# Kernel optimization log

Measured on AMD Instinct MI355X. Metric: run time of the kernel, lower is better.

## Reference

```python
import jax, jax.numpy as jnp
from jax import lax
import numpy as np

N, K, F, H, NG, T = 32768, 16, 64, 128, 1024, 2


def setup_inputs() -> dict:
    key = jax.random.key(0)
    ks = jax.random.split(key, 24)
    def rn(k, shape, s=0.05):
        return jax.random.normal(k, shape, jnp.float32) * s
    inp = {
        'n': jax.random.normal(ks[0], (N, F), jnp.float32),
        'nbr': jax.random.randint(ks[1], (N, K), 0, N),
        # deterministic sorted graph ids -> every graph non-empty (safe segment_max)
        'gid': (jnp.arange(N) * NG) // N,
        'G': NG,
        # SAGEConv layer 1: LSTM(F,F), fc_self/fc_neigh F->H
        'lstm1_Wih': rn(ks[2], (F, 4 * F)), 'lstm1_Whh': rn(ks[3], (F, 4 * F)), 'lstm1_b': jnp.zeros((4 * F,), jnp.float32),
        'fcs1_W': rn(ks[4], (F, H)), 'fcs1_b': jnp.zeros((H,), jnp.float32),
        'fcn1_W': rn(ks[5], (F, H)), 'fcn1_b': jnp.zeros((H,), jnp.float32),
        # SAGEConv layer 2: LSTM(H,H), fc_self/fc_neigh H->H
        'lstm2_Wih': rn(ks[6], (H, 4 * H)), 'lstm2_Whh': rn(ks[7], (H, 4 * H)), 'lstm2_b': jnp.zeros((4 * H,), jnp.float32),
        'fcs2_W': rn(ks[8], (H, H)), 'fcs2_b': jnp.zeros((H,), jnp.float32),
        'fcn2_W': rn(ks[9], (H, H)), 'fcn2_b': jnp.zeros((H,), jnp.float32),
        # WeightedSumAndMax atom weighting: H->1
        'rw_W': rn(ks[10], (H, 1)), 'rw_b': jnp.zeros((1,), jnp.float32),
        # task head: 2H->H, H->T
        'h1_W': rn(ks[11], (2 * H, H)), 'h1_b': jnp.zeros((H,), jnp.float32),
        'h2_W': rn(ks[12], (H, T)), 'h2_b': jnp.zeros((T,), jnp.float32),
    }
    return inp


def _lstm_last(xseq, Wih, Whh, b):
    # xseq: [N, K, Fin]; returns last hidden state [N, Hh]
    Hh = Whh.shape[0]
    h0 = jnp.zeros((xseq.shape[0], Hh), xseq.dtype)
    def step(carry, xt):
        h, c = carry
        g = xt @ Wih + h @ Whh + b  # [N, 4H], torch gate order i,f,g,o
        i, f, gg, o = jnp.split(g, 4, axis=-1)
        c = jax.nn.sigmoid(f) * c + jax.nn.sigmoid(i) * jnp.tanh(gg)
        h = jax.nn.sigmoid(o) * jnp.tanh(c)
        return (h, c), None
    (h, _), _ = lax.scan(step, (h0, h0), jnp.swapaxes(xseq, 0, 1))
    return h


def _sage_layer(x, nbr, Wih, Whh, b, Ws, bs, Wn, bn):
    hn = _lstm_last(x[nbr], Wih, Whh, b)          # LSTM aggregate of neighbors
    return jax.nn.sigmoid(x @ Ws + bs + hn @ Wn + bn)


def reference(n, nbr, gid, G,
              lstm1_Wih, lstm1_Whh, lstm1_b, fcs1_W, fcs1_b, fcn1_W, fcn1_b,
              lstm2_Wih, lstm2_Whh, lstm2_b, fcs2_W, fcs2_b, fcn2_W, fcn2_b,
              rw_W, rw_b, h1_W, h1_b, h2_W, h2_b):
    G = int(G)
    h1 = _sage_layer(n, nbr, lstm1_Wih, lstm1_Whh, lstm1_b, fcs1_W, fcs1_b, fcn1_W, fcn1_b)
    h2 = _sage_layer(h1, nbr, lstm2_Wih, lstm2_Whh, lstm2_b, fcs2_W, fcs2_b, fcn2_W, fcn2_b)
    # WeightedSumAndMax readout
    w = jax.nn.sigmoid(h2 @ rw_W + rw_b)                       # [N,1]
    wsum = jax.ops.segment_sum(w * h2, gid, num_segments=G)    # [G,H]
    mx = jax.ops.segment_max(h2, gid, num_segments=G)          # [G,H]
    gemb = jnp.concatenate([wsum, mx], axis=-1)                # [G,2H]
    y = jax.nn.sigmoid(gemb @ h1_W + h1_b)
    y = jax.nn.sigmoid(y @ h2_W + h2_b)                        # classification
    return y
```

## Files before the change

kernel.cpp:

```cpp
#include <hip/hip_runtime.h>

typedef unsigned short u16;
typedef __attribute__((ext_vector_type(8))) short bf16x8;
typedef __attribute__((ext_vector_type(4))) float f32x4;
typedef __attribute__((ext_vector_type(2))) float f32x2;

constexpr int N_ = 32768;
constexpr int H_ = 128;
constexpr int G_ = 1024;
constexpr int T_ = 2;

__device__ __forceinline__ float sigf(float x){
  float e = __builtin_amdgcn_exp2f(x * -1.44269504f);
  return __builtin_amdgcn_rcpf(1.0f + e);
}
__device__ __forceinline__ f32x2 sig2p(f32x2 xp){
  f32x2 e; e.x = __builtin_amdgcn_exp2f(xp.x); e.y = __builtin_amdgcn_exp2f(xp.y);
  f32x2 d = e + 1.0f;
  float r = __builtin_amdgcn_rcpf(d.x * d.y);
  return (f32x2){r * d.y, r * d.x};
}
__device__ __forceinline__ f32x2 tanh2p(f32x2 xp){
  f32x2 e; e.x = __builtin_amdgcn_exp2f(xp.x); e.y = __builtin_amdgcn_exp2f(xp.y);
  f32x2 d = e + 1.0f;
  float r = __builtin_amdgcn_rcpf(d.x * d.y);
  f32x2 rr = (f32x2){r * d.y, r * d.x};
  return 1.0f - 2.0f*rr;
}
__device__ __forceinline__ f32x2 tanh2(f32x2 x){
  f32x2 t = x * 2.88539008f;
  f32x2 e; e.x = __builtin_amdgcn_exp2f(t.x); e.y = __builtin_amdgcn_exp2f(t.y);
  f32x2 d = e + 1.0f;
  float r = __builtin_amdgcn_rcpf(d.x * d.y);
  f32x2 rr = (f32x2){r * d.y, r * d.x};
  return 1.0f - 2.0f*rr;
}
__device__ __forceinline__ u16 f2bf(float f){
  unsigned u = __float_as_uint(f);
  unsigned r = (u + 0x7FFFu + ((u>>16)&1u))>>16;
  return (u16)r;
}
__device__ __forceinline__ unsigned cvt_pk_bf16(float a, float b){
  unsigned r;
  asm("v_cvt_pk_bf16_f32 %0, %1, %2" : "=v"(r) : "v"(a), "v"(b));
  return r;
}
__device__ __forceinline__ float bf2f(u16 h){ return __uint_as_float(((unsigned)h)<<16); }
__device__ __forceinline__ float asf(unsigned u){ return __uint_as_float(u); }
__device__ __forceinline__ f32x4 mfma16(bf16x8 a, bf16x8 b, f32x4 c){
  return __builtin_amdgcn_mfma_f32_16x16x32_bf16(a,b,c,0,0,0);
}

__global__ __launch_bounds__(64)
void pack_all(const float* __restrict__ l1Wih, const float* __restrict__ fcs1W,
              const float* __restrict__ l1Whh, const float* __restrict__ fcn1W,
              const float* __restrict__ l2Wih, const float* __restrict__ fcs2W,
              const float* __restrict__ l2Whh, const float* __restrict__ fcn2W,
              const float* __restrict__ l1b, const float* __restrict__ bs1,
              const float* __restrict__ bn1,
              const float* __restrict__ l2b, const float* __restrict__ bs2,
              const float* __restrict__ bn2,
              u16* BY1, u16* BW1, u16* BN1, u16* BY2, u16* BW2, u16* BN2,
              u16* bY1, u16* bY2)
{
  int b = blockIdx.x;
  const int lane = threadIdx.x;
  if (b == 416) {
    for (int i = lane; i < 1024; i += 64) {
      if (i < 384) {
        int p = i; float v;
        if (p < 256) {
          int o = (p&3)*64 + ((p>>6)<<4) + ((p>>2)&15);
          float sc = ((p&3)==2) ? 2.88539008f : -1.44269504f;
          v = l1b[o]*sc;
        } else { int j = p-256; v = bs1[j] + bn1[j]; }
        bY1[p] = f2bf(v);
      } else {
        int p = i - 384; float v;
        if (p < 512) {
          int o = (p&3)*128 + ((p>>6)<<4) + ((p>>2)&15);
          float sc = ((p&3)==2) ? 2.88539008f : -1.44269504f;
          v = l2b[o]*sc;
        } else { int j = p-512; v = bs2[j] + bn2[j]; }
        bY2[p] = f2bf(v);
      }
    }
    return;
  }
  const float* src; u16* dst; int srcNC, NTtot, ntOff, ntCnt, Fh, perm;
  if      (b < 32)  { src=l1Wih; dst=BY1; srcNC=256; NTtot=24; ntOff=0;  ntCnt=16; Fh=64;  perm=2; }
  else if (b < 48)  { src=fcs1W; dst=BY1; srcNC=128; NTtot=24; ntOff=16; ntCnt=8;  Fh=0;   perm=0; b-=32; }
  else if (b < 80)  { src=l1Whh; dst=BW1; srcNC=256; NTtot=16; ntOff=0;  ntCnt=16; Fh=64;  perm=1; b-=48; }
  else if (b < 96)  { src=fcn1W; dst=BN1; srcNC=128; NTtot=8;  ntOff=0;  ntCnt=8;  Fh=0;   perm=0; b-=80; }
  else if (b < 224) { src=l2Wih; dst=BY2; srcNC=512; NTtot=40; ntOff=0;  ntCnt=32; Fh=128; perm=2; b-=96; }
  else if (b < 256) { src=fcs2W; dst=BY2; srcNC=128; NTtot=40; ntOff=32; ntCnt=8;  Fh=0;   perm=0; b-=224; }
  else if (b < 384) { src=l2Whh; dst=BW2; srcNC=512; NTtot=32; ntOff=0;  ntCnt=32; Fh=128; perm=1; b-=256; }
  else              { src=fcn2W; dst=BN2; srcNC=128; NTtot=8;  ntOff=0;  ntCnt=8;  Fh=0;   perm=0; b-=384; }
  const int ntl = b % ntCnt, kt = b / ntCnt;
  const int n = lane & 15, qq = lane >> 4;
  int pr = ntl*16 + n;
  int o; float scale = 1.0f;
  if (perm == 1) {
    int g = (pr>>4)&3;
    o = g*Fh + ((pr>>6)<<4) + (pr&15);
    scale = (g==2) ? 2.88539008f : -1.44269504f;
  } else if (perm == 2) {
    int g = pr&3;
    o = g*Fh + ((pr>>6)<<4) + ((pr>>2)&15);
    scale = (g==2) ? 2.88539008f : -1.44269504f;
  } else o = pr;
  u16* d = dst + ((size_t)((kt*NTtot + ntOff + ntl)*64 + lane))*8;
#pragma unroll
  for (int j = 0; j < 8; ++j) {
    int k = kt*32 + qq*8 + j;
    d[j] = f2bf(src[(size_t)k*srcNC + o] * scale);
  }
}

template<int KT, int NTT, int AF32>
__global__ __launch_bounds__(256, 2)
void gemm_kernel(const void* __restrict__ Ain,
                 const u16* __restrict__ Bpk,
                 const u16* __restrict__ biasbf,
                 u16* __restrict__ out, int out_stride)
{
  constexpr int KA  = KT*32;
  constexpr int NTW = NTT/4;
  constexpr int STR = KA + 8;
  __shared__ __align__(16) u16 a_lds[32*STR];
  const int tid  = threadIdx.x;
  const int base = blockIdx.x*32;
  {
    const int sub = tid & 7, rowl = tid >> 3;
    if constexpr (AF32) {
      const float* src = (const float*)Ain + (size_t)(base+rowl)*KA;
#pragma unroll
      for (int cc = 0; cc < KA/32; ++cc) {
        int e0 = (cc*8+sub)*4;
        float4 v = *(const float4*)(src + e0);
        ushort4 bv;
        bv.x = f2bf(v.x); bv.y = f2bf(v.y); bv.z = f2bf(v.z); bv.w = f2bf(v.w);
        *(ushort4*)(void*)(a_lds + rowl*STR + e0) = bv;
      }
    } else {
      const u16* src = (const u16*)Ain + (size_t)(base+rowl)*KA;
#pragma unroll
      for (int cc = 0; cc < KA/64; ++cc) {
        int e0 = (cc*8+sub)*8;
        uint4 v = *(const uint4*)(const void*)(src + e0);
        *(uint4*)(void*)(a_lds + rowl*STR + e0) = v;
      }
    }
  }
  __syncthreads();
  const int lane = tid & 63, w = tid >> 6;
  const int lc = lane & 15, q = lane >> 4;
  f32x4 acc[2][NTW];
  f32x4 z = {0.f,0.f,0.f,0.f};
#pragma unroll
  for (int m = 0; m < 2; ++m)
#pragma unroll
    for (int j = 0; j < NTW; ++j) acc[m][j] = z;
#pragma unroll
  for (int kt = 0; kt < KT; ++kt) {
    bf16x8 af0 = *(const bf16x8*)(const void*)(a_lds + lc*STR      + kt*32 + q*8);
    bf16x8 af1 = *(const bf16x8*)(const void*)(a_lds + (lc+16)*STR + kt*32 + q*8);
#pragma unroll
    for (int j = 0; j < NTW; ++j) {
      bf16x8 bf = *(const bf16x8*)(const void*)(Bpk + ((size_t)((kt*NTT + w*NTW + j)*64 + lane))*8);
      acc[0][j] = mfma16(af0, bf, acc[0][j]);
      acc[1][j] = mfma16(af1, bf, acc[1][j]);
    }
  }
#pragma unroll
  for (int m = 0; m < 2; ++m)
#pragma unroll
    for (int j = 0; j < NTW; ++j) {
      int col = (w*NTW + j)*16 + lc;
#pragma unroll
      for (int r = 0; r < 4; ++r) {
        int row = base + m*16 + q*4 + r;
        out[(size_t)row*out_stride + col] = f2bf(acc[m][j][r] + bf2f(biasbf[col]));
      }
    }
}

template<int KT, int MW>
__global__ __launch_bounds__(KT*128, MW)
void lstm_kernel(const int* __restrict__ nbr,
                 const u16* __restrict__ Y, int nctot,
                 const u16* __restrict__ Bpk,
                 const u16* __restrict__ BN,
                 const u16* __restrict__ Sp, int s_stride, int s_coloff,
                 u16* __restrict__ out)
{
  constexpr int F   = KT*32;
  constexpr int NW  = KT*2;
  constexpr int NTT = KT*8;
  constexpr int STR = F + 8;
  __shared__ __align__(16) u16 h_lds[2][16*STR];
  __shared__ int nbr_s[256];
  const int tid  = threadIdx.x;
  const int base = blockIdx.x * 16;
  const int lane = tid & 63, w = tid >> 6;
  const int lc = lane & 15, q = lane >> 4;

  for (int i = tid; i < 256; i += NW*64) nbr_s[i] = nbr[base*16 + i];

  bf16x8 bfr[KT][4];
#pragma unroll
  for (int kt = 0; kt < KT; ++kt)
#pragma unroll
    for (int g = 0; g < 4; ++g)
      bfr[kt][g] = *(const bf16x8*)(const void*)(Bpk + ((size_t)((kt*NTT + w*4 + g)*64 + lane))*8);

  f32x2 cs[2];
  cs[0] = (f32x2){0.f,0.f}; cs[1] = (f32x2){0.f,0.f};
  __syncthreads();

  const char* Yb = (const char*)Y;
  const unsigned rowbytes = (unsigned)nctot * 2u;
  const unsigned lanebyte = (unsigned)(w*64 + lc*4) * 2u;
  const int wcol = w*16 + lc;

  uint2 yv[4];
#pragma unroll
  for (int r = 0; r < 4; ++r) {
    unsigned vr = (unsigned)nbr_s[(q*4 + r)*16];
    yv[r] = *(const uint2*)(const void*)(Yb + (vr*rowbytes + lanebyte));
  }

  for (int t = 0; t < 16; ++t) {
    const u16* hr = h_lds[t & 1];
    u16*       hw = h_lds[(t & 1) ^ 1];
    f32x4 acc[4];
#pragma unroll
    for (int r = 0; r < 4; ++r) {
      acc[0][r] = asf(yv[r].x << 16);
      acc[1][r] = asf(yv[r].x & 0xffff0000u);
      acc[2][r] = asf(yv[r].y << 16);
      acc[3][r] = asf(yv[r].y & 0xffff0000u);
    }
    if (t < 15) {
#pragma unroll
      for (int r = 0; r < 4; ++r) {
        unsigned vr = (unsigned)nbr_s[(q*4 + r)*16 + t + 1];
        yv[r] = *(const uint2*)(const void*)(Yb + (vr*rowbytes + lanebyte));
      }
    }
    if (t != 0) {
#pragma unroll
      for (int kt = 0; kt < KT; ++kt) {
        bf16x8 af = *(const bf16x8*)(const void*)(hr + lc*STR + kt*32 + q*8);
#pragma unroll
        for (int g = 0; g < 4; ++g) acc[g] = mfma16(af, bfr[kt][g], acc[g]);
      }
    }
#pragma unroll
    for (int rp = 0; rp < 2; ++rp) {
      f32x2 gi = (f32x2){acc[0][2*rp], acc[0][2*rp+1]};
      f32x2 gf = (f32x2){acc[1][2*rp], acc[1][2*rp+1]};
      f32x2 gg = (f32x2){acc[2][2*rp], acc[2][2*rp+1]};
      f32x2 go = (f32x2){acc[3][2*rp], acc[3][2*rp+1]};
      f32x2 c  = sig2p(gf)*cs[rp] + sig2p(gi)*tanh2p(gg);
      cs[rp] = c;
      f32x2 hh = sig2p(go)*tanh2(c);
      unsigned pkd = cvt_pk_bf16(hh.x, hh.y);
      int r0 = q*4 + 2*rp;
      hw[r0*STR + wcol]     = (u16)pkd;
      hw[(r0+1)*STR + wcol] = (u16)(pkd >> 16);
    }
    __syncthreads();
  }

  constexpr int CPW = 8 / NW;
  const u16* hf = h_lds[0];
#pragma unroll
  for (int cc2 = 0; cc2 < CPW; ++cc2) {
    const int nt = w*CPW + cc2;
    f32x4 a2 = {0.f,0.f,0.f,0.f};
#pragma unroll
    for (int kt = 0; kt < KT; ++kt) {
      bf16x8 nf = *(const bf16x8*)(const void*)(BN + ((size_t)((kt*8 + nt)*64 + lane))*8);
      bf16x8 af = *(const bf16x8*)(const void*)(hf + lc*STR + kt*32 + q*8);
      a2 = mfma16(af, nf, a2);
    }
    const int col = nt*16 + lc;
#pragma unroll
    for (int r = 0; r < 4; ++r) {
      int row = base + q*4 + r;
      float v = a2[r] + bf2f(Sp[(size_t)row*s_stride + s_coloff + col]);
      out[(size_t)row*H_ + col] = f2bf(sigf(v));
    }
  }
}

__global__ __launch_bounds__(256, 6)
void lstm1_y2(const int* __restrict__ nbr,
              const u16* __restrict__ Y1,
              const u16* __restrict__ Bpk,
              const u16* __restrict__ BN,
              const u16* __restrict__ BY2,
              const u16* __restrict__ bY2,
              u16* __restrict__ Y2)
{
  constexpr int STR = 72;
  __shared__ __align__(16) u16 h_lds[2][16*STR];
  __shared__ __align__(16) u16 hs[16*136];
  __shared__ int nbr_s[256];
  const int tid  = threadIdx.x;
  const int base = blockIdx.x * 16;
  const int lane = tid & 63, w = tid >> 6;
  const int lc = lane & 15, q = lane >> 4;

  nbr_s[tid] = nbr[base*16 + tid];

  bf16x8 bfr[2][4];
#pragma unroll
  for (int kt = 0; kt < 2; ++kt)
#pragma unroll
    for (int g = 0; g < 4; ++g)
      bfr[kt][g] = *(const bf16x8*)(const void*)(Bpk + ((size_t)((kt*16 + w*4 + g)*64 + lane))*8);

  f32x2 cs[2];
  cs[0] = (f32x2){0.f,0.f}; cs[1] = (f32x2){0.f,0.f};
  __syncthreads();

  const char* Yb = (const char*)Y1;
  const unsigned lanebyte = (unsigned)(w*64 + lc*4) * 2u;
  const int wcol = w*16 + lc;

  uint2 yv[4];
#pragma unroll
  for (int r = 0; r < 4; ++r) {
    unsigned vr = (unsigned)nbr_s[(q*4 + r)*16];
    yv[r] = *(const uint2*)(const void*)(Yb + (vr*768u + lanebyte));
  }

  for (int t = 0; t < 16; ++t) {
    const u16* hr = h_lds[t & 1];
    u16*       hw = h_lds[(t & 1) ^ 1];
    f32x4 acc[4];
#pragma unroll
    for (int r = 0; r < 4; ++r) {
      acc[0][r] = asf(yv[r].x << 16);
      acc[1][r] = asf(yv[r].x & 0xffff0000u);
      acc[2][r] = asf(yv[r].y << 16);
      acc[3][r] = asf(yv[r].y & 0xffff0000u);
    }
    if (t < 15) {
#pragma unroll
      for (int r = 0; r < 4; ++r) {
        unsigned vr = (unsigned)nbr_s[(q*4 + r)*16 + t + 1];
        yv[r] = *(const uint2*)(const void*)(Yb + (vr*768u + lanebyte));
      }
    }
    if (t != 0) {
#pragma unroll
      for (int kt = 0; kt < 2; ++kt) {
        bf16x8 af = *(const bf16x8*)(const void*)(hr + lc*STR + kt*32 + q*8);
#pragma unroll
        for (int g = 0; g < 4; ++g) acc[g] = mfma16(af, bfr[kt][g], acc[g]);
      }
    }
#pragma unroll
    for (int rp = 0; rp < 2; ++rp) {
      f32x2 gi = (f32x2){acc[0][2*rp], acc[0][2*rp+1]};
      f32x2 gf = (f32x2){acc[1][2*rp], acc[1][2*rp+1]};
      f32x2 gg = (f32x2){acc[2][2*rp], acc[2][2*rp+1]};
      f32x2 go = (f32x2){acc[3][2*rp], acc[3][2*rp+1]};
      f32x2 c  = sig2p(gf)*cs[rp] + sig2p(gi)*tanh2p(gg);
      cs[rp] = c;
      f32x2 hh = sig2p(go)*tanh2(c);
      unsigned pkd = cvt_pk_bf16(hh.x, hh.y);
      int r0 = q*4 + 2*rp;
      hw[r0*STR + wcol]     = (u16)pkd;
      hw[(r0+1)*STR + wcol] = (u16)(pkd >> 16);
    }
    __syncthreads();
  }

  const u16* hf = h_lds[0];
#pragma unroll
  for (int cc2 = 0; cc2 < 2; ++cc2) {
    const int nt = w*2 + cc2;
    f32x4 a2 = {0.f,0.f,0.f,0.f};
#pragma unroll
    for (int kt = 0; kt < 2; ++kt) {
      bf16x8 nf = *(const bf16x8*)(const void*)(BN + ((size_t)((kt*8 + nt)*64 + lane))*8);
      bf16x8 af = *(const bf16x8*)(const void*)(hf + lc*STR + kt*32 + q*8);
      a2 = mfma16(af, nf, a2);
    }
    const int col = nt*16 + lc;
#pragma unroll
    for (int r = 0; r < 4; ++r) {
      int row = base + q*4 + r;
      float v = a2[r] + bf2f(Y1[(size_t)row*384 + 256 + col]);
      hs[(q*4 + r)*136 + col] = f2bf(sigf(v));
    }
  }
  __syncthreads();

#pragma unroll
  for (int j = 0; j < 10; ++j) {
    const int nt = w*10 + j;
    const int col = nt*16 + lc;
    float bv = bf2f(bY2[col]);
    f32x4 acc;
#pragma unroll
    for (int r = 0; r < 4; ++r) acc[r] = bv;
#pragma unroll
    for (int kt = 0; kt < 4; ++kt) {
      bf16x8 af = *(const bf16x8*)(const void*)(hs + lc*136 + kt*32 + q*8);
      bf16x8 bf = *(const bf16x8*)(const void*)(BY2 + ((size_t)((kt*40 + nt)*64 + lane))*8);
      acc = mfma16(af, bf, acc);
    }
#pragma unroll
    for (int r = 0; r < 4; ++r)
      Y2[(size_t)(base + q*4 + r)*640 + col] = f2bf(acc[r]);
  }
}

__global__ __launch_bounds__(128)
void head_kernel(const u16* __restrict__ h2, const float* __restrict__ rwW,
                 const float* __restrict__ rwb,
                 const float* __restrict__ h1W, const float* __restrict__ h1b,
                 const float* __restrict__ h2W, const float* __restrict__ h2b,
                 float* __restrict__ out)
{
  __shared__ float h2s[32*H_];
  __shared__ float part[32*4];
  __shared__ float wv[32];
  __shared__ float gemb[2*H_];
  __shared__ float y1[H_];
  const int g = blockIdx.x, t = threadIdx.x;
  for (int r = 0; r < 32; ++r)
    h2s[r*H_ + t] = bf2f(h2[(size_t)(g*32 + r)*H_ + t]);
  __syncthreads();
  { int r = t>>2, qq = t&3; float p = 0.f;
    for (int h = qq*32; h < qq*32+32; ++h) p += h2s[r*H_+h]*rwW[h];
    part[r*4+qq] = p; }
  __syncthreads();
  if (t < 32) wv[t] = sigf(part[t*4]+part[t*4+1]+part[t*4+2]+part[t*4+3]+rwb[0]);
  __syncthreads();
  { float wsum=0.f, mx=-3.402823466e38f;
    for (int r = 0; r < 32; ++r) { float v = h2s[r*H_+t]; wsum += wv[r]*v; mx = fmaxf(mx,v); }
    gemb[t]=wsum; gemb[H_+t]=mx; }
  __syncthreads();
  { float a = h1b[t];
    for (int k = 0; k < 2*H_; ++k) a += gemb[k]*h1W[k*H_+t];
    y1[t]=sigf(a); }
  __syncthreads();
  if (t < T_) {
    float a = h2b[t];
    for (int h = 0; h < H_; ++h) a += y1[h]*h2W[h*T_+t];
    out[(size_t)g*T_+t] = sigf(a);
  }
}

extern "C" void kernel_launch(void* const* d_in, const int* in_sizes, int n_in,
                              void* d_out, int out_size, void* d_ws, size_t ws_size,
                              hipStream_t stream) {
  const float* n_feat = (const float*)d_in[0];
  const int*   nbr    = (const int*)d_in[1];
  const float* l1Wih = (const float*)d_in[4];
  const float* l1Whh = (const float*)d_in[5];
  const float* l1b   = (const float*)d_in[6];
  const float* fcs1W = (const float*)d_in[7];
  const float* fcs1b = (const float*)d_in[8];
  const float* fcn1W = (const float*)d_in[9];
  const float* fcn1b = (const float*)d_in[10];
  const float* l2Wih = (const float*)d_in[11];
  const float* l2Whh = (const float*)d_in[12];
  const float* l2b   = (const float*)d_in[13];
  const float* fcs2W = (const float*)d_in[14];
  const float* fcs2b = (const float*)d_in[15];
  const float* fcn2W = (const float*)d_in[16];
  const float* fcn2b = (const float*)d_in[17];
  const float* rwW   = (const float*)d_in[18];
  const float* rwb   = (const float*)d_in[19];
  const float* h1W   = (const float*)d_in[20];
  const float* h1b   = (const float*)d_in[21];
  const float* h2W   = (const float*)d_in[22];
  const float* h2b   = (const float*)d_in[23];

  char* ws = (char*)d_ws;

  if (ws_size >= 67600000) {
    u16* Y1 = (u16*)(ws);
    u16* Y2 = (u16*)(ws + 25165824);
    u16* h2 = (u16*)(ws);
    char* wt = ws + 67108864;
    u16* BY1 = (u16*)(wt);
    u16* BW1 = (u16*)(wt + 49152);
    u16* BN1 = (u16*)(wt + 81920);
    u16* BY2 = (u16*)(wt + 98304);
    u16* BW2 = (u16*)(wt + 262144);
    u16* BN2 = (u16*)(wt + 393216);
    u16* bY1 = (u16*)(wt + 425984);
    u16* bY2 = (u16*)(wt + 426752);

    pack_all<<<417, 64, 0, stream>>>(l1Wih, fcs1W, l1Whh, fcn1W,
                                     l2Wih, fcs2W, l2Whh, fcn2W,
                                     l1b, fcs1b, fcn1b, l2b, fcs2b, fcn2b,
                                     BY1, BW1, BN1, BY2, BW2, BN2, bY1, bY2);
    gemm_kernel<2,24,1><<<1024, 256, 0, stream>>>(n_feat, BY1, bY1, Y1, 384);
    lstm1_y2<<<2048, 256, 0, stream>>>(nbr, Y1, BW1, BN1, BY2, bY2, Y2);
    lstm_kernel<4,4><<<2048, 512, 0, stream>>>(nbr, Y2, 640, BW2, BN2, Y2, 640, 512, h2);
    head_kernel<<<G_, 128, 0, stream>>>(h2, rwW, rwb, h1W, h1b, h2W, h2b, (float*)d_out);
  } else {
    u16* Y   = (u16*)(ws);
    u16* h1  = (u16*)(ws + 41943040);
    u16* h2  = (u16*)(ws + 50331648);
    char* wt = ws + 58720256;
    u16* BY1 = (u16*)(wt);
    u16* BW1 = (u16*)(wt + 49152);
    u16* BN1 = (u16*)(wt + 81920);
    u16* BY2 = (u16*)(wt + 98304);
    u16* BW2 = (u16*)(wt + 262144);
    u16* BN2 = (u16*)(wt + 393216);
    u16* bY1 = (u16*)(wt + 425984);
    u16* bY2 = (u16*)(wt + 426752);

    pack_all<<<417, 64, 0, stream>>>(l1Wih, fcs1W, l1Whh, fcn1W,
                                     l2Wih, fcs2W, l2Whh, fcn2W,
                                     l1b, fcs1b, fcn1b, l2b, fcs2b, fcn2b,
                                     BY1, BW1, BN1, BY2, BW2, BN2, bY1, bY2);
    gemm_kernel<2,24,1><<<1024, 256, 0, stream>>>(n_feat, BY1, bY1, Y, 384);
    lstm_kernel<2,6><<<2048, 256, 0, stream>>>(nbr, Y, 384, BW1, BN1, Y, 384, 256, h1);
    gemm_kernel<4,40,0><<<1024, 256, 0, stream>>>(h1, BY2, bY2, Y, 640);
    lstm_kernel<4,4><<<2048, 512, 0, stream>>>(nbr, Y, 640, BW2, BN2, Y, 640, 512, h2);
    head_kernel<<<G_, 128, 0, stream>>>(h2, rwW, rwb, h1W, h1b, h2W, h2b, (float*)d_out);
  }
}
```

Before: 282.1 us.

## Fuse layer-2 LSTM aggregation with graph readout and head into one kernel

Replaces the separate layer-2 LSTM kernel and the head kernel with one kernel. Each 512-thread block processes 32 nodes, which is exactly one graph given the sorted graph ids, and runs two 16-row MFMA tiles per wave. The block keeps h2 in LDS and performs the weighted-sum/max readout and MLP head in place, removing the h2 global write/read and one launch. The trade-off is half as many blocks and doubled per-block register and LDS use, which may lower occupancy or latency hiding. It also relies on each graph being exactly 32 contiguous nodes.

```diff
diff --git a/kernel.cpp b/kernel.cpp
--- a/kernel.cpp
+++ b/kernel.cpp
@@ -185,6 +185,301 @@
     }
 }
 
+__global__ __launch_bounds__(256, 6)
+void lstm1_y2(const int* __restrict__ nbr,
+              const u16* __restrict__ Y1,
+              const u16* __restrict__ Bpk,
+              const u16* __restrict__ BN,
+              const u16* __restrict__ BY2,
+              const u16* __restrict__ bY2,
+              u16* __restrict__ Y2)
+{
+  constexpr int STR = 72;
+  __shared__ __align__(16) u16 h_lds[2][16*STR];
+  __shared__ __align__(16) u16 hs[16*136];
+  __shared__ int nbr_s[256];
+  const int tid  = threadIdx.x;
+  const int base = blockIdx.x * 16;
+  const int lane = tid & 63, w = tid >> 6;
+  const int lc = lane & 15, q = lane >> 4;
+
+  nbr_s[tid] = nbr[base*16 + tid];
+
+  bf16x8 bfr[2][4];
+#pragma unroll
+  for (int kt = 0; kt < 2; ++kt)
+#pragma unroll
+    for (int g = 0; g < 4; ++g)
+      bfr[kt][g] = *(const bf16x8*)(const void*)(Bpk + ((size_t)((kt*16 + w*4 + g)*64 + lane))*8);
+
+  f32x2 cs[2];
+  cs[0] = (f32x2){0.f,0.f}; cs[1] = (f32x2){0.f,0.f};
+  __syncthreads();
+
+  const char* Yb = (const char*)Y1;
+  const unsigned lanebyte = (unsigned)(w*64 + lc*4) * 2u;
+  const int wcol = w*16 + lc;
+
+  uint2 yv[4];
+#pragma unroll
+  for (int r = 0; r < 4; ++r) {
+    unsigned vr = (unsigned)nbr_s[(q*4 + r)*16];
+    yv[r] = *(const uint2*)(const void*)(Yb + (vr*768u + lanebyte));
+  }
+
+  for (int t = 0; t < 16; ++t) {
+    const u16* hr = h_lds[t & 1];
+    u16*       hw = h_lds[(t & 1) ^ 1];
+    f32x4 acc[4];
+#pragma unroll
+    for (int r = 0; r < 4; ++r) {
+      acc[0][r] = asf(yv[r].x << 16);
+      acc[1][r] = asf(yv[r].x & 0xffff0000u);
+      acc[2][r] = asf(yv[r].y << 16);
+      acc[3][r] = asf(yv[r].y & 0xffff0000u);
+    }
+    if (t < 15) {
+#pragma unroll
+      for (int r = 0; r < 4; ++r) {
+        unsigned vr = (unsigned)nbr_s[(q*4 + r)*16 + t + 1];
+        yv[r] = *(const uint2*)(const void*)(Yb + (vr*768u + lanebyte));
+      }
+    }
+    if (t != 0) {
+#pragma unroll
+      for (int kt = 0; kt < 2; ++kt) {
+        bf16x8 af = *(const bf16x8*)(const void*)(hr + lc*STR + kt*32 + q*8);
+#pragma unroll
+        for (int g = 0; g < 4; ++g) acc[g] = mfma16(af, bfr[kt][g], acc[g]);
+      }
+    }
+#pragma unroll
+    for (int rp = 0; rp < 2; ++rp) {
+      f32x2 gi = (f32x2){acc[0][2*rp], acc[0][2*rp+1]};
+      f32x2 gf = (f32x2){acc[1][2*rp], acc[1][2*rp+1]};
+      f32x2 gg = (f32x2){acc[2][2*rp], acc[2][2*rp+1]};
+      f32x2 go = (f32x2){acc[3][2*rp], acc[3][2*rp+1]};
+      f32x2 c  = sig2p(gf)*cs[rp] + sig2p(gi)*tanh2p(gg);
+      cs[rp] = c;
+      f32x2 hh = sig2p(go)*tanh2(c);
+      unsigned pkd = cvt_pk_bf16(hh.x, hh.y);
+      int r0 = q*4 + 2*rp;
+      hw[r0*STR + wcol]     = (u16)pkd;
+      hw[(r0+1)*STR + wcol] = (u16)(pkd >> 16);
+    }
+    __syncthreads();
+  }
+
+  const u16* hf = h_lds[0];
+#pragma unroll
+  for (int cc2 = 0; cc2 < 2; ++cc2) {
+    const int nt = w*2 + cc2;
+    f32x4 a2 = {0.f,0.f,0.f,0.f};
+#pragma unroll
+    for (int kt = 0; kt < 2; ++kt) {
+      bf16x8 nf = *(const bf16x8*)(const void*)(BN + ((size_t)((kt*8 + nt)*64 + lane))*8);
+      bf16x8 af = *(const bf16x8*)(const void*)(hf + lc*STR + kt*32 + q*8);
+      a2 = mfma16(af, nf, a2);
+    }
+    const int col = nt*16 + lc;
+#pragma unroll
+    for (int r = 0; r < 4; ++r) {
+      int row = base + q*4 + r;
+      float v = a2[r] + bf2f(Y1[(size_t)row*384 + 256 + col]);
+      hs[(q*4 + r)*136 + col] = f2bf(sigf(v));
+    }
+  }
+  __syncthreads();
+
+#pragma unroll
+  for (int j = 0; j < 10; ++j) {
+    const int nt = w*10 + j;
+    const int col = nt*16 + lc;
+    float bv = bf2f(bY2[col]);
+    f32x4 acc;
+#pragma unroll
+    for (int r = 0; r < 4; ++r) acc[r] = bv;
+#pragma unroll
+    for (int kt = 0; kt < 4; ++kt) {
+      bf16x8 af = *(const bf16x8*)(const void*)(hs + lc*136 + kt*32 + q*8);
+      bf16x8 bf = *(const bf16x8*)(const void*)(BY2 + ((size_t)((kt*40 + nt)*64 + lane))*8);
+      acc = mfma16(af, bf, acc);
+    }
+#pragma unroll
+    for (int r = 0; r < 4; ++r)
+      Y2[(size_t)(base + q*4 + r)*640 + col] = f2bf(acc[r]);
+  }
+}
+
+__global__ __launch_bounds__(512, 4)
+void lstm2_head(const int* __restrict__ nbr,
+                const u16* __restrict__ Y, int nctot,
+                const u16* __restrict__ Bpk,
+                const u16* __restrict__ BN,
+                const u16* __restrict__ Sp, int s_stride, int s_coloff,
+                const float* __restrict__ rwW, const float* __restrict__ rwb,
+                const float* __restrict__ h1W, const float* __restrict__ h1b,
+                const float* __restrict__ h2W, const float* __restrict__ h2b,
+                float* __restrict__ out)
+{
+  constexpr int KT  = 4;
+  constexpr int NW  = 8;
+  constexpr int NTT = 32;
+  constexpr int STR = 136;
+  __shared__ __align__(16) u16 h_lds[2][32*STR];
+  __shared__ int nbr_s[512];
+  __shared__ float part[128];
+  __shared__ float wv_s[32];
+  __shared__ float gemb[256];
+  __shared__ float y1[128];
+  const int tid  = threadIdx.x;
+  const int base = blockIdx.x * 32;
+  const int lane = tid & 63, w = tid >> 6;
+  const int lc = lane & 15, q = lane >> 4;
+
+  for (int i = tid; i < 512; i += NW*64) nbr_s[i] = nbr[base*16 + i];
+
+  bf16x8 bfr[KT][4];
+#pragma unroll
+  for (int kt = 0; kt < KT; ++kt)
+#pragma unroll
+    for (int g = 0; g < 4; ++g)
+      bfr[kt][g] = *(const bf16x8*)(const void*)(Bpk + ((size_t)((kt*NTT + w*4 + g)*64 + lane))*8);
+
+  f32x2 cs[2][2];
+#pragma unroll
+  for (int m = 0; m < 2; ++m)
+#pragma unroll
+    for (int rp = 0; rp < 2; ++rp) cs[m][rp] = (f32x2){0.f, 0.f};
+  __syncthreads();
+
+  const char* Yb = (const char*)Y;
+  const unsigned rowbytes = (unsigned)nctot * 2u;
+  const unsigned lanebyte = (unsigned)(w*64 + lc*4) * 2u;
+  const int wcol = w*16 + lc;
+
+  uint2 yv[2][4];
+#pragma unroll
+  for (int m = 0; m < 2; ++m)
+#pragma unroll
+    for (int r = 0; r < 4; ++r) {
+      unsigned vr = (unsigned)nbr_s[(m*16 + q*4 + r)*16];
+      yv[m][r] = *(const uint2*)(const void*)(Yb + (vr*rowbytes + lanebyte));
+    }
+
+  for (int t = 0; t < 16; ++t) {
+    const u16* hr = h_lds[t & 1];
+    u16*       hw = h_lds[(t & 1) ^ 1];
+#pragma unroll
+    for (int m = 0; m < 2; ++m) {
+      f32x4 acc[4];
+#pragma unroll
+      for (int r = 0; r < 4; ++r) {
+        acc[0][r] = asf(yv[m][r].x << 16);
+        acc[1][r] = asf(yv[m][r].x & 0xffff0000u);
+        acc[2][r] = asf(yv[m][r].y << 16);
+        acc[3][r] = asf(yv[m][r].y & 0xffff0000u);
+      }
+      if (t < 15) {
+#pragma unroll
+        for (int r = 0; r < 4; ++r) {
+          unsigned vr = (unsigned)nbr_s[(m*16 + q*4 + r)*16 + t + 1];
+          yv[m][r] = *(const uint2*)(const void*)(Yb + (vr*rowbytes + lanebyte));
+        }
+      }
+      if (t != 0) {
+#pragma unroll
+        for (int kt = 0; kt < KT; ++kt) {
+          bf16x8 af = *(const bf16x8*)(const void*)(hr + (lc + m*16)*STR + kt*32 + q*8);
+#pragma unroll
+          for (int g = 0; g < 4; ++g) acc[g] = mfma16(af, bfr[kt][g], acc[g]);
+        }
+      }
+#pragma unroll
+      for (int rp = 0; rp < 2; ++rp) {
+        f32x2 gi = (f32x2){acc[0][2*rp], acc[0][2*rp+1]};
+        f32x2 gf = (f32x2){acc[1][2*rp], acc[1][2*rp+1]};
+        f32x2 gg = (f32x2){acc[2][2*rp], acc[2][2*rp+1]};
+        f32x2 go = (f32x2){acc[3][2*rp], acc[3][2*rp+1]};
+        f32x2 c  = sig2p(gf)*cs[m][rp] + sig2p(gi)*tanh2p(gg);
+        cs[m][rp] = c;
+        f32x2 hh = sig2p(go)*tanh2(c);
+        unsigned pkd = cvt_pk_bf16(hh.x, hh.y);
+        int r0 = m*16 + q*4 + 2*rp;
+        hw[r0*STR + wcol]     = (u16)pkd;
+        hw[(r0+1)*STR + wcol] = (u16)(pkd >> 16);
+      }
+    }
+    __syncthreads();
+  }
+
+  const u16* hf = h_lds[0];
+  u16* hs = h_lds[1];
+  {
+    const int nt = w;
+    f32x4 a2[2];
+    a2[0] = (f32x4){0.f,0.f,0.f,0.f};
+    a2[1] = (f32x4){0.f,0.f,0.f,0.f};
+#pragma unroll
+    for (int kt = 0; kt < KT; ++kt) {
+      bf16x8 nf = *(const bf16x8*)(const void*)(BN + ((size_t)((kt*8 + nt)*64 + lane))*8);
+#pragma unroll
+      for (int m = 0; m < 2; ++m) {
+        bf16x8 af = *(const bf16x8*)(const void*)(hf + (lc + m*16)*STR + kt*32 + q*8);
+        a2[m] = mfma16(af, nf, a2[m]);
+      }
+    }
+    const int col = nt*16 + lc;
+#pragma unroll
+    for (int m = 0; m < 2; ++m)
+#pragma unroll
+      for (int r = 0; r < 4; ++r) {
+        int rl = m*16 + q*4 + r;
+        float v = a2[m][r] + bf2f(Sp[(size_t)(base + rl)*s_stride + s_coloff + col]);
+        hs[rl*STR + col] = f2bf(sigf(v));
+      }
+  }
+  __syncthreads();
+
+  if (tid < 128) {
+    int r = tid >> 2, qq = tid & 3;
+    float p = 0.f;
+    for (int h = qq*32; h < qq*32 + 32; ++h) p += bf2f(hs[r*STR + h]) * rwW[h];
+    part[tid] = p;
+  }
+  __syncthreads();
+  if (tid < 32)
+    wv_s[tid] = sigf(part[tid*4] + part[tid*4+1] + part[tid*4+2] + part[tid*4+3] + rwb[0]);
+  __syncthreads();
+
+  if (tid < 128) {
+    float wsum = 0.f, mx = -3.402823466e38f;
+    for (int r = 0; r < 32; ++r) {
+      float v = bf2f(hs[r*STR + tid]);
+      wsum += wv_s[r] * v;
+      mx = fmaxf(mx, v);
+    }
+    gemb[tid] = wsum;
+    y1[tid] = mx;
+  }
+  __syncthreads();
+  if (tid < 128) gemb[128 + tid] = y1[tid];
+  __syncthreads();
+
+  if (tid < 128) {
+    float a = h1b[tid];
+    for (int k = 0; k < 256; ++k) a += gemb[k] * h1W[k*H_ + tid];
+    y1[tid] = sigf(a);
+  }
+  __syncthreads();
+
+  if (tid < T_) {
+    float a = h2b[tid];
+    for (int h = 0; h < H_; ++h) a += y1[h] * h2W[h*T_ + tid];
+    out[(size_t)blockIdx.x*T_ + tid] = sigf(a);
+  }
+}
+
 template<int KT, int MW>
 __global__ __launch_bounds__(KT*128, MW)
 void lstm_kernel(const int* __restrict__ nbr,
@@ -292,169 +587,6 @@
       float v = a2[r] + bf2f(Sp[(size_t)row*s_stride + s_coloff + col]);
       out[(size_t)row*H_ + col] = f2bf(sigf(v));
     }
-  }
-}
-
-__global__ __launch_bounds__(256, 6)
-void lstm1_y2(const int* __restrict__ nbr,
-              const u16* __restrict__ Y1,
-              const u16* __restrict__ Bpk,
-              const u16* __restrict__ BN,
-              const u16* __restrict__ BY2,
-              const u16* __restrict__ bY2,
-              u16* __restrict__ Y2)
-{
-  constexpr int STR = 72;
-  __shared__ __align__(16) u16 h_lds[2][16*STR];
-  __shared__ __align__(16) u16 hs[16*136];
-  __shared__ int nbr_s[256];
-  const int tid  = threadIdx.x;
-  const int base = blockIdx.x * 16;
-  const int lane = tid & 63, w = tid >> 6;
-  const int lc = lane & 15, q = lane >> 4;
-
-  nbr_s[tid] = nbr[base*16 + tid];
-
-  bf16x8 bfr[2][4];
-#pragma unroll
-  for (int kt = 0; kt < 2; ++kt)
-#pragma unroll
-    for (int g = 0; g < 4; ++g)
-      bfr[kt][g] = *(const bf16x8*)(const void*)(Bpk + ((size_t)((kt*16 + w*4 + g)*64 + lane))*8);
-
-  f32x2 cs[2];
-  cs[0] = (f32x2){0.f,0.f}; cs[1] = (f32x2){0.f,0.f};
-  __syncthreads();
-
-  const char* Yb = (const char*)Y1;
-  const unsigned lanebyte = (unsigned)(w*64 + lc*4) * 2u;
-  const int wcol = w*16 + lc;
-
-  uint2 yv[4];
-#pragma unroll
-  for (int r = 0; r < 4; ++r) {
-    unsigned vr = (unsigned)nbr_s[(q*4 + r)*16];
-    yv[r] = *(const uint2*)(const void*)(Yb + (vr*768u + lanebyte));
-  }
-
-  for (int t = 0; t < 16; ++t) {
-    const u16* hr = h_lds[t & 1];
-    u16*       hw = h_lds[(t & 1) ^ 1];
-    f32x4 acc[4];
-#pragma unroll
-    for (int r = 0; r < 4; ++r) {
-      acc[0][r] = asf(yv[r].x << 16);
-      acc[1][r] = asf(yv[r].x & 0xffff0000u);
-      acc[2][r] = asf(yv[r].y << 16);
-      acc[3][r] = asf(yv[r].y & 0xffff0000u);
-    }
-    if (t < 15) {
-#pragma unroll
-      for (int r = 0; r < 4; ++r) {
-        unsigned vr = (unsigned)nbr_s[(q*4 + r)*16 + t + 1];
-        yv[r] = *(const uint2*)(const void*)(Yb + (vr*768u + lanebyte));
-      }
-    }
-    if (t != 0) {
-#pragma unroll
-      for (int kt = 0; kt < 2; ++kt) {
-        bf16x8 af = *(const bf16x8*)(const void*)(hr + lc*STR + kt*32 + q*8);
-#pragma unroll
-        for (int g = 0; g < 4; ++g) acc[g] = mfma16(af, bfr[kt][g], acc[g]);
-      }
-    }
-#pragma unroll
-    for (int rp = 0; rp < 2; ++rp) {
-      f32x2 gi = (f32x2){acc[0][2*rp], acc[0][2*rp+1]};
-      f32x2 gf = (f32x2){acc[1][2*rp], acc[1][2*rp+1]};
-      f32x2 gg = (f32x2){acc[2][2*rp], acc[2][2*rp+1]};
-      f32x2 go = (f32x2){acc[3][2*rp], acc[3][2*rp+1]};
-      f32x2 c  = sig2p(gf)*cs[rp] + sig2p(gi)*tanh2p(gg);
-      cs[rp] = c;
-      f32x2 hh = sig2p(go)*tanh2(c);
-      unsigned pkd = cvt_pk_bf16(hh.x, hh.y);
-      int r0 = q*4 + 2*rp;
-      hw[r0*STR + wcol]     = (u16)pkd;
-      hw[(r0+1)*STR + wcol] = (u16)(pkd >> 16);
-    }
-    __syncthreads();
-  }
-
-  const u16* hf = h_lds[0];
-#pragma unroll
-  for (int cc2 = 0; cc2 < 2; ++cc2) {
-    const int nt = w*2 + cc2;
-    f32x4 a2 = {0.f,0.f,0.f,0.f};
-#pragma unroll
-    for (int kt = 0; kt < 2; ++kt) {
-      bf16x8 nf = *(const bf16x8*)(const void*)(BN + ((size_t)((kt*8 + nt)*64 + lane))*8);
-      bf16x8 af = *(const bf16x8*)(const void*)(hf + lc*STR + kt*32 + q*8);
-      a2 = mfma16(af, nf, a2);
-    }
-    const int col = nt*16 + lc;
-#pragma unroll
-    for (int r = 0; r < 4; ++r) {
-      int row = base + q*4 + r;
-      float v = a2[r] + bf2f(Y1[(size_t)row*384 + 256 + col]);
-      hs[(q*4 + r)*136 + col] = f2bf(sigf(v));
-    }
-  }
-  __syncthreads();
-
-#pragma unroll
-  for (int j = 0; j < 10; ++j) {
-    const int nt = w*10 + j;
-    const int col = nt*16 + lc;
-    float bv = bf2f(bY2[col]);
-    f32x4 acc;
-#pragma unroll
-    for (int r = 0; r < 4; ++r) acc[r] = bv;
-#pragma unroll
-    for (int kt = 0; kt < 4; ++kt) {
-      bf16x8 af = *(const bf16x8*)(const void*)(hs + lc*136 + kt*32 + q*8);
-      bf16x8 bf = *(const bf16x8*)(const void*)(BY2 + ((size_t)((kt*40 + nt)*64 + lane))*8);
-      acc = mfma16(af, bf, acc);
-    }
-#pragma unroll
-    for (int r = 0; r < 4; ++r)
-      Y2[(size_t)(base + q*4 + r)*640 + col] = f2bf(acc[r]);
-  }
-}
-
-__global__ __launch_bounds__(128)
-void head_kernel(const u16* __restrict__ h2, const float* __restrict__ rwW,
-                 const float* __restrict__ rwb,
-                 const float* __restrict__ h1W, const float* __restrict__ h1b,
-                 const float* __restrict__ h2W, const float* __restrict__ h2b,
-                 float* __restrict__ out)
-{
-  __shared__ float h2s[32*H_];
-  __shared__ float part[32*4];
-  __shared__ float wv[32];
-  __shared__ float gemb[2*H_];
-  __shared__ float y1[H_];
-  const int g = blockIdx.x, t = threadIdx.x;
-  for (int r = 0; r < 32; ++r)
-    h2s[r*H_ + t] = bf2f(h2[(size_t)(g*32 + r)*H_ + t]);
-  __syncthreads();
-  { int r = t>>2, qq = t&3; float p = 0.f;
-    for (int h = qq*32; h < qq*32+32; ++h) p += h2s[r*H_+h]*rwW[h];
-    part[r*4+qq] = p; }
-  __syncthreads();
-  if (t < 32) wv[t] = sigf(part[t*4]+part[t*4+1]+part[t*4+2]+part[t*4+3]+rwb[0]);
-  __syncthreads();
-  { float wsum=0.f, mx=-3.402823466e38f;
-    for (int r = 0; r < 32; ++r) { float v = h2s[r*H_+t]; wsum += wv[r]*v; mx = fmaxf(mx,v); }
-    gemb[t]=wsum; gemb[H_+t]=mx; }
-  __syncthreads();
-  { float a = h1b[t];
-    for (int k = 0; k < 2*H_; ++k) a += gemb[k]*h1W[k*H_+t];
-    y1[t]=sigf(a); }
-  __syncthreads();
-  if (t < T_) {
-    float a = h2b[t];
-    for (int h = 0; h < H_; ++h) a += y1[h]*h2W[h*T_+t];
-    out[(size_t)g*T_+t] = sigf(a);
   }
 }
 
@@ -489,7 +621,6 @@
   if (ws_size >= 67600000) {
     u16* Y1 = (u16*)(ws);
     u16* Y2 = (u16*)(ws + 25165824);
-    u16* h2 = (u16*)(ws);
     char* wt = ws + 67108864;
     u16* BY1 = (u16*)(wt);
     u16* BW1 = (u16*)(wt + 49152);
@@ -506,13 +637,13 @@
                                      BY1, BW1, BN1, BY2, BW2, BN2, bY1, bY2);
     gemm_kernel<2,24,1><<<1024, 256, 0, stream>>>(n_feat, BY1, bY1, Y1, 384);
     lstm1_y2<<<2048, 256, 0, stream>>>(nbr, Y1, BW1, BN1, BY2, bY2, Y2);
-    lstm_kernel<4,4><<<2048, 512, 0, stream>>>(nbr, Y2, 640, BW2, BN2, Y2, 640, 512, h2);
-    head_kernel<<<G_, 128, 0, stream>>>(h2, rwW, rwb, h1W, h1b, h2W, h2b, (float*)d_out);
+    lstm2_head<<<1024, 512, 0, stream>>>(nbr, Y2, 640, BW2, BN2, Y2, 640, 512,
+                                         rwW, rwb, h1W, h1b, h2W, h2b,
+                                         (float*)d_out);
   } else {
     u16* Y   = (u16*)(ws);
     u16* h1  = (u16*)(ws + 41943040);
-    u16* h2  = (u16*)(ws + 50331648);
-    char* wt = ws + 58720256;
+    char* wt = ws + 50331648;
     u16* BY1 = (u16*)(wt);
     u16* BW1 = (u16*)(wt + 49152);
     u16* BN1 = (u16*)(wt + 81920);
@@ -529,7 +660,8 @@
     gemm_kernel<2,24,1><<<1024, 256, 0, stream>>>(n_feat, BY1, bY1, Y, 384);
     lstm_kernel<2,6><<<2048, 256, 0, stream>>>(nbr, Y, 384, BW1, BN1, Y, 384, 256, h1);
     gemm_kernel<4,40,0><<<1024, 256, 0, stream>>>(h1, BY2, bY2, Y, 640);
-    lstm_kernel<4,4><<<2048, 512, 0, stream>>>(nbr, Y, 640, BW2, BN2, Y, 640, 512, h2);
-    head_kernel<<<G_, 128, 0, stream>>>(h2, rwW, rwb, h1W, h1b, h2W, h2b, (float*)d_out);
-  }
-}
+    lstm2_head<<<1024, 512, 0, stream>>>(nbr, Y, 640, BW2, BN2, Y, 640, 512,
+                                         rwW, rwb, h1W, h1b, h2W, h2b,
+                                         (float*)d_out);
+  }
+}
```

After: 280.4 us. No clear change (-0.6%).
